# Kernel optimization log

Hardware: AMD Instinct MI355X
Metric: run time of the kernel (lower is better)

Reference implementation:

```python
import jax, jax.numpy as jnp
import numpy as np

G = 128          # voxel grid extent per axis
KS = 3           # kernel size per axis
KK = KS ** 3     # 27 kernel offsets
N_IN, N_OUT, C_IN, C_OUT = 50000, 100000, 128, 128


def setup_inputs() -> dict:
    key = jax.random.key(0)
    k1, k2, k3, k4 = jax.random.split(key, 4)
    features = jax.random.normal(k1, (N_IN, C_IN), dtype=jnp.float32)
    W = jax.random.normal(k2, (KK, C_IN, C_OUT), dtype=jnp.float32) * (1.0 / np.sqrt(C_IN * KK))
    inp_positions = jax.random.randint(k3, (N_IN, 3), 0, G, dtype=jnp.int32)
    out_positions = jax.random.randint(k4, (N_OUT, 3), 0, G, dtype=jnp.int32)
    return {"features": features, "W": W,
            "inp_positions": inp_positions, "out_positions": out_positions}


def _kernel_offsets():
    r = np.arange(KS) - KS // 2  # [-1, 0, 1] for KS=3 (offset=0 since KS is odd)
    dx, dy, dz = np.meshgrid(r, r, r, indexing="ij")
    return jnp.asarray(np.stack([dx.ravel(), dy.ravel(), dz.ravel()], axis=1), dtype=jnp.int32)  # [KK,3]


def reference(features, W, inp_positions, out_positions):
    # Sparse conv-transpose: voxelize input points (voxel_size=1, offset=0 -> identity
    # on integer coords), build voxel->input-index hash (dense grid table), then for
    # each output point gather the input feature at each of the KK kernel offsets and
    # accumulate W[k'] @ feat with mirrored kernel index (transpose of SparseConv).
    lin_in = (inp_positions[:, 0] * G + inp_positions[:, 1]) * G + inp_positions[:, 2]
    grid = jnp.full((G * G * G,), -1, dtype=jnp.int32)
    grid = grid.at[lin_in].max(jnp.arange(N_IN, dtype=jnp.int32))  # deterministic on dup voxels

    offsets = _kernel_offsets()          # [KK, 3]
    W_mirror = W[::-1]                   # transpose conv uses mirrored kernel index

    def step(acc, xk):
        off, Wk = xk                     # off [3], Wk [C_IN, C_OUT]
        nb = out_positions + off[None, :]               # [N_OUT, 3]
        in_bounds = jnp.all((nb >= 0) & (nb < G), axis=1)
        lin = (nb[:, 0] * G + nb[:, 1]) * G + nb[:, 2]
        idx = grid[jnp.clip(lin, 0, G * G * G - 1)]      # [N_OUT]
        ok = in_bounds & (idx >= 0)
        f = jnp.where(ok[:, None], features[jnp.clip(idx, 0)], 0.0)  # [N_OUT, C_IN]
        return acc + f @ Wk, None

    acc0 = jnp.zeros((out_positions.shape[0], W.shape[2]), dtype=features.dtype)
    out, _ = jax.lax.scan(step, acc0, (offsets, W_mirror))
    return out
```

## Files before the change

### kernel.cpp

```cpp
#include <hip/hip_runtime.h>
#include <hip/hip_bf16.h>

#define G    128
#define GGG  (G * G * G)
#define C    128
#define KK   27
#define CAP  4096
#define RT   16

typedef __attribute__((ext_vector_type(8))) short bf16x8;
typedef __attribute__((ext_vector_type(4))) float f32x4;

__device__ __forceinline__ ushort f2b(float f) {
    __hip_bfloat16 h = __float2bfloat16(f);
    return *reinterpret_cast<ushort*>(&h);
}

__global__ void prep_kernel(uint4* __restrict__ grid16_4, int* __restrict__ cnt,
                            const float* __restrict__ W, ushort* __restrict__ Wtb) {
    int tid = blockIdx.x * blockDim.x + threadIdx.x;
    int stride = gridDim.x * blockDim.x;
    uint4 ffff = {0xFFFFFFFFu, 0xFFFFFFFFu, 0xFFFFFFFFu, 0xFFFFFFFFu};
    for (int i = tid; i < GGG * 2 / 16; i += stride) grid16_4[i] = ffff;
    if (tid < KK) cnt[tid] = 0;
    const int NW = KK * C * C;
    for (int i = tid; i < NW; i += stride) {
        int m = i >> 14;
        int r = i & 16383;
        int co = r >> 7, ci = r & 127;
        Wtb[i] = f2b(W[(size_t)(KK - 1 - m) * C * C + ci * C + co]);
    }
}

__global__ void scatter16_kernel(const int* __restrict__ pos,
                                 unsigned int* __restrict__ gword, int n) {
    int i = blockIdx.x * blockDim.x + threadIdx.x;
    if (i >= n) return;
    int x = pos[3 * i], y = pos[3 * i + 1], z = pos[3 * i + 2];
    int lin = (x * G + y) * G + z;
    unsigned int* w = &gword[lin >> 1];
    int sh = (lin & 1) * 16;
    unsigned int val = (unsigned int)i;
    unsigned int old = *w, assumed;
    do {
        unsigned int cur = (old >> sh) & 0xFFFFu;
        if (cur != 0xFFFFu && cur >= val) break;
        unsigned int nw = (old & ~(0xFFFFu << sh)) | (val << sh);
        assumed = old;
        old = atomicCAS(w, assumed, nw);
    } while (old != assumed);
}

__global__ __launch_bounds__(256) void compact4_kernel(
    const int* __restrict__ out_pos, const ushort* __restrict__ grid16,
    int* __restrict__ cnt, int2* __restrict__ pairs,
    int* __restrict__ cnt_row, int* __restrict__ rowtap, int n_out)
{
    int row = blockIdx.x * 256 + threadIdx.x;
    bool valid = row < n_out;
    int lane = threadIdx.x & 63;

    int px = 0, py = 0, pz = 0;
    if (valid) { px = out_pos[3*row]; py = out_pos[3*row+1]; pz = out_pos[3*row+2]; }

    int idx[KK];
#pragma unroll
    for (int m = 0; m < KK; ++m) {
        int x = px + m / 9 - 1, y = py + (m % 9) / 3 - 1, z = pz + m % 3 - 1;
        bool inb = valid && (unsigned)x < G && (unsigned)y < G && (unsigned)z < G;
        int v = inb ? (int)grid16[(x * G + y) * G + z] : 0xFFFF;
        idx[m] = (v == 0xFFFF) ? -1 : v;
    }

    __shared__ int bcnt[KK], bbase[KK];
    if (threadIdx.x < KK) bcnt[threadIdx.x] = 0;
    __syncthreads();

    int gl[KK];
#pragma unroll
    for (int m = 0; m < KK; ++m) {
        unsigned long long act = __ballot(idx[m] >= 0);
        int lpre = __popcll(act & ((1ull << lane) - 1ull));
        int wcnt = __popcll(act);
        int wbase = 0;
        if (lane == 0 && wcnt) wbase = atomicAdd(&bcnt[m], wcnt);
        wbase = __shfl(wbase, 0);
        gl[m] = wbase + lpre;
    }
    __syncthreads();
    if (threadIdx.x < KK) bbase[threadIdx.x] = atomicAdd(&cnt[threadIdx.x], bcnt[threadIdx.x]);
    __syncthreads();

    int gs[KK];
    int cr = 0;
#pragma unroll
    for (int m = 0; m < KK; ++m) {
        int g = -1;
        if (idx[m] >= 0) {
            g = bbase[m] + gl[m];
            if (g >= CAP) g = -1;
        }
        gs[m] = g;
        if (g >= 0) ++cr;
    }

    int dest = (cr == 1) ? row : -1;
    int k = 0;
#pragma unroll
    for (int m = 0; m < KK; ++m) {
        int g = gs[m];
        if (g >= 0) {
            pairs[m * CAP + g] = make_int2(idx[m], dest);
            if (k < RT) { rowtap[k * n_out + row] = (g << 5) | m; ++k; }
        }
    }
    if (valid) cnt_row[row] = cr;
}

__global__ __launch_bounds__(256, 3) void pair_mm4_kernel(
    const float* __restrict__ features, const ushort* __restrict__ Wtb,
    const int2* __restrict__ pairs, const int* __restrict__ cnt,
    ushort* __restrict__ part, float* __restrict__ out)
{
    int m = blockIdx.y;
    int nm = min(cnt[m], CAP);
    if ((int)(blockIdx.x * 64) >= nm) return;

    __shared__ ushort Wl[128 * 136];
    __shared__ ushort Af[64 * 136];
    __shared__ int    idx_s[64];
    __shared__ int    dest_s[64];

    {
        const uint4* src = (const uint4*)(Wtb + (size_t)m * C * C);
        uint4* dst = (uint4*)Wl;
        for (int q = threadIdx.x; q < 2048; q += 256) {
            int r = q >> 4, c = q & 15;
            dst[r * 17 + c] = src[q];
        }
    }

    int lane = threadIdx.x & 63;
    int w    = threadIdx.x >> 6;
    int l15  = lane & 15;
    int quad = lane >> 4;
    const float4* fg4 = (const float4*)features;

    for (int base = blockIdx.x * 64; base < nm; base += gridDim.x * 64) {
        __syncthreads();
        if (threadIdx.x < 64) {
            int g = base + threadIdx.x;
            int2 pr = (g < nm) ? pairs[m * CAP + g] : make_int2(-1, -1);
            idx_s[threadIdx.x]  = pr.x;
            dest_s[threadIdx.x] = pr.y;
        }
        __syncthreads();

#pragma unroll
        for (int k = 0; k < 8; ++k) {
            int q = threadIdx.x + k * 256;
            int r = q >> 5, c4 = q & 31;
            int id = idx_s[r];
            if (id >= 0) {
                float4 v = fg4[(size_t)id * 32 + c4];
                union { ushort u[4]; uint2 p; } pk;
                pk.u[0] = f2b(v.x); pk.u[1] = f2b(v.y);
                pk.u[2] = f2b(v.z); pk.u[3] = f2b(v.w);
                *(uint2*)&Af[r * 136 + c4 * 4] = pk.p;
            }
        }
        __syncthreads();

        f32x4 acc[8];
#pragma unroll
        for (int n = 0; n < 8; ++n) acc[n] = (f32x4){0.f, 0.f, 0.f, 0.f};

        int arow = 16 * w + l15;
#pragma unroll
        for (int kk = 0; kk < 4; ++kk) {
            bf16x8 a = *(bf16x8*)&Af[arow * 136 + kk * 32 + quad * 8];
#pragma unroll
            for (int n = 0; n < 8; ++n) {
                bf16x8 b = *(bf16x8*)&Wl[(n * 16 + l15) * 136 + kk * 32 + quad * 8];
                acc[n] = __builtin_amdgcn_mfma_f32_16x16x32_bf16(a, b, acc[n], 0, 0, 0);
            }
        }

        int r0 = 16 * w + quad * 4;
#pragma unroll
        for (int reg = 0; reg < 4; ++reg) {
            int r = r0 + reg;
            if (base + r >= nm) continue;
            int d = dest_s[r];
            if (d >= 0) {
                float* o = out + (size_t)d * C + l15;
#pragma unroll
                for (int n = 0; n < 8; ++n) o[n * 16] = acc[n][reg];
            } else {
                ushort* p = part + ((size_t)(m * CAP + base + r)) * C + l15;
#pragma unroll
                for (int n = 0; n < 8; ++n) p[n * 16] = f2b(acc[n][reg]);
            }
        }
    }
}

__global__ __launch_bounds__(256) void gather_sum3_kernel(
    const ushort* __restrict__ part, const int* __restrict__ rowtap,
    const int* __restrict__ cnt_row, float* __restrict__ out, int n_out)
{
    int row0 = blockIdx.x * 16;
    int rl = threadIdx.x >> 4;
    int t  = threadIdx.x & 15;
    int row = row0 + rl;

    __shared__ int rt_s[RT][16];
    __shared__ int cnt_s[16];
    __shared__ int maxc;
    if (threadIdx.x < 16) {
        int r = row0 + threadIdx.x;
        cnt_s[threadIdx.x] = (r < n_out) ? cnt_row[r] : 0;
    }
    __syncthreads();
    if (threadIdx.x == 0) {
        int mx = 0;
#pragma unroll
        for (int i = 0; i < 16; ++i) mx = max(mx, cnt_s[i]);
        maxc = mx;
    }
    __syncthreads();
    {
        int k = threadIdx.x >> 4, r = threadIdx.x & 15;
        if (k < maxc)
            rt_s[k][r] = (row0 + r < n_out) ? rowtap[k * n_out + row0 + r] : 0;
    }
    __syncthreads();

    int nt = cnt_s[rl];
    if (nt == 1) return;

    float acc[8] = {0,0,0,0,0,0,0,0};
    for (int k = 0; k < nt; ++k) {
        int e = rt_s[k][rl];
        int m = e & 31, g = e >> 5;
        uint4 v = *(const uint4*)(part + ((size_t)(m * CAP + g)) * C + t * 8);
        acc[0] += __uint_as_float(v.x << 16);
        acc[1] += __uint_as_float(v.x & 0xffff0000u);
        acc[2] += __uint_as_float(v.y << 16);
        acc[3] += __uint_as_float(v.y & 0xffff0000u);
        acc[4] += __uint_as_float(v.z << 16);
        acc[5] += __uint_as_float(v.z & 0xffff0000u);
        acc[6] += __uint_as_float(v.w << 16);
        acc[7] += __uint_as_float(v.w & 0xffff0000u);
    }
    if (row < n_out) {
        float* o = out + (size_t)row * C + t * 8;
        *(float4*)(o)     = (float4){acc[0], acc[1], acc[2], acc[3]};
        *(float4*)(o + 4) = (float4){acc[4], acc[5], acc[6], acc[7]};
    }
}

__global__ void init2_kernel(int4* __restrict__ grid4, int* __restrict__ cnt) {
    int i = blockIdx.x * blockDim.x + threadIdx.x;
    int stride = gridDim.x * blockDim.x;
    int4 mone = {-1, -1, -1, -1};
    for (int j = i; j < GGG / 4; j += stride) grid4[j] = mone;
    if (i < KK) cnt[i] = 0;
}

__global__ void scatter_kernel(const int* __restrict__ pos,
                               int* __restrict__ grid, int n) {
    int i = blockIdx.x * blockDim.x + threadIdx.x;
    if (i >= n) return;
    int x = pos[3 * i], y = pos[3 * i + 1], z = pos[3 * i + 2];
    atomicMax(&grid[(x * G + y) * G + z], i);
}

__global__ __launch_bounds__(128) void gather_mm_kernel(
    const float* __restrict__ features, const float* __restrict__ W,
    const int* __restrict__ out_pos, const int* __restrict__ grid,
    float* __restrict__ out, int n_out)
{
    int row = blockIdx.x;
    if (row >= n_out) return;
    int c = threadIdx.x;
    __shared__ int   nb_idx[KK];
    __shared__ float feat_s[C];
    int px = out_pos[3*row], py = out_pos[3*row+1], pz = out_pos[3*row+2];
    if (c < KK) {
        int i = c / 9, j = (c % 9) / 3, k = c % 3;
        int x = px + i - 1, y = py + j - 1, z = pz + k - 1;
        int idx = -1;
        if ((unsigned)x < G && (unsigned)y < G && (unsigned)z < G)
            idx = grid[(x * G + y) * G + z];
        nb_idx[c] = idx;
    }
    __syncthreads();
    float acc = 0.f;
    for (int m = 0; m < KK; ++m) {
        int idx = nb_idx[m];
        if (idx < 0) continue;
        __syncthreads();
        feat_s[c] = features[idx * C + c];
        __syncthreads();
        const float* __restrict__ Wk = W + (KK - 1 - m) * C * C + c;
        float a = 0.f;
#pragma unroll
        for (int ci = 0; ci < C; ++ci) a += feat_s[ci] * Wk[ci * C];
        acc += a;
    }
    out[row * C + c] = acc;
}

extern "C" void kernel_launch(void* const* d_in, const int* in_sizes, int n_in,
                              void* d_out, int out_size, void* d_ws, size_t ws_size,
                              hipStream_t stream) {
    const float* features = (const float*)d_in[0];
    const float* W        = (const float*)d_in[1];
    const int*   inp_pos  = (const int*)d_in[2];
    const int*   out_pos  = (const int*)d_in[3];
    float*       out      = (float*)d_out;

    int n_in_pts  = in_sizes[2] / 3;
    int n_out_pts = out_size / C;

    size_t o_grid   = 0;
    size_t o_cnt    = (size_t)GGG * 4;
    size_t o_pairs  = (o_cnt + 256 + 255) & ~(size_t)255;
    size_t o_cntr   = (o_pairs + (size_t)KK * CAP * 8 + 255) & ~(size_t)255;
    size_t o_rowtap = (o_cntr + (size_t)n_out_pts * 4 + 255) & ~(size_t)255;
    size_t o_wtb    = (o_rowtap + (size_t)RT * n_out_pts * 4 + 255) & ~(size_t)255;
    size_t o_part   = (o_wtb + (size_t)KK * C * C * 2 + 255) & ~(size_t)255;
    size_t need     = o_part + (size_t)KK * CAP * C * 2;

    ushort* grid16  = (ushort*)((char*)d_ws + o_grid);
    int*    cnt     = (int*)((char*)d_ws + o_cnt);
    int2*   pairs   = (int2*)((char*)d_ws + o_pairs);
    int*    cnt_row = (int*)((char*)d_ws + o_cntr);
    int*    rowtap  = (int*)((char*)d_ws + o_rowtap);
    ushort* Wtb     = (ushort*)((char*)d_ws + o_wtb);
    ushort* part    = (ushort*)((char*)d_ws + o_part);

    if (ws_size < need) {
        int* grid32 = (int*)d_ws;
        hipLaunchKernelGGL(init2_kernel, dim3(2048), dim3(256), 0, stream,
                           (int4*)grid32, cnt);
        hipLaunchKernelGGL(scatter_kernel, dim3((n_in_pts + 255) / 256), dim3(256), 0, stream,
                           inp_pos, grid32, n_in_pts);
        hipLaunchKernelGGL(gather_mm_kernel, dim3(n_out_pts), dim3(128), 0, stream,
                           features, W, out_pos, grid32, out, n_out_pts);
        return;
    }

    hipLaunchKernelGGL(prep_kernel, dim3(1024), dim3(256), 0, stream,
                       (uint4*)grid16, cnt, W, Wtb);
    hipLaunchKernelGGL(scatter16_kernel, dim3((n_in_pts + 255) / 256), dim3(256), 0, stream,
                       inp_pos, (unsigned int*)grid16, n_in_pts);
    hipLaunchKernelGGL(compact4_kernel, dim3((n_out_pts + 255) / 256), dim3(256), 0, stream,
                       out_pos, grid16, cnt, pairs, cnt_row, rowtap, n_out_pts);
    hipLaunchKernelGGL(pair_mm4_kernel, dim3(40, KK), dim3(256), 0, stream,
                       features, Wtb, pairs, cnt, part, out);
    hipLaunchKernelGGL(gather_sum3_kernel, dim3((n_out_pts + 15) / 16), dim3(256), 0, stream,
                       part, rowtap, cnt_row, out, n_out_pts);
}
```

Baseline: 141.3 us.

## Pre-convert features to bf16, tile W transpose via LDS, double pair-matmul rows

The prep kernel now transposes W through a shared-memory tile with coalesced reads and writes, and converts all input features to a bf16 copy in workspace. The pair matmul gathers these bf16 rows directly with 16-byte loads and processes 128 pairs per block, with two 16-row MFMA sub-tiles per wave sharing each B fragment. This halves the gather bytes per pair and raises MFMA reuse of the W tile. The cost is a full extra pass over the features, more workspace, doubled LDS per block, and lower occupancy (launch bounds cut from 3 to 2 blocks).

```diff
diff --git a/kernel.cpp b/kernel.cpp
--- a/kernel.cpp
+++ b/kernel.cpp
@@ -16,19 +16,51 @@
     return *reinterpret_cast<ushort*>(&h);
 }
 
-__global__ void prep_kernel(uint4* __restrict__ grid16_4, int* __restrict__ cnt,
-                            const float* __restrict__ W, ushort* __restrict__ Wtb) {
-    int tid = blockIdx.x * blockDim.x + threadIdx.x;
-    int stride = gridDim.x * blockDim.x;
+#define WT_BLOCKS 108
+__global__ __launch_bounds__(256) void prep5_kernel(
+    uint4* __restrict__ grid16_4, int* __restrict__ cnt,
+    const float* __restrict__ W, ushort* __restrict__ Wtb,
+    const float4* __restrict__ fg4, uint2* __restrict__ fb2, int nf4)
+{
+    if (blockIdx.x < WT_BLOCKS) {
+        int mm = blockIdx.x >> 2;
+        int t  = blockIdx.x & 3;
+        __shared__ float Ls[32][129];
+        const float* src = W + (size_t)mm * C * C + (size_t)(t * 32) * C;
+#pragma unroll
+        for (int k = 0; k < 16; ++k) {
+            int q = threadIdx.x + k * 256;
+            int r = q >> 7, co = q & 127;
+            Ls[r][co] = src[r * C + co];
+        }
+        __syncthreads();
+        ushort* dst = Wtb + (size_t)(KK - 1 - mm) * C * C + t * 32;
+#pragma unroll
+        for (int k = 0; k < 4; ++k) {
+            int q = threadIdx.x + k * 256;
+            int co = q >> 3, j = q & 7;
+            union { ushort u[4]; uint2 p; } pk;
+            pk.u[0] = f2b(Ls[4*j+0][co]);
+            pk.u[1] = f2b(Ls[4*j+1][co]);
+            pk.u[2] = f2b(Ls[4*j+2][co]);
+            pk.u[3] = f2b(Ls[4*j+3][co]);
+            *(uint2*)&dst[co * C + 4 * j] = pk.p;
+        }
+        return;
+    }
+    int b = blockIdx.x - WT_BLOCKS;
+    int nb = gridDim.x - WT_BLOCKS;
+    int tid = b * 256 + threadIdx.x;
+    int stride = nb * 256;
     uint4 ffff = {0xFFFFFFFFu, 0xFFFFFFFFu, 0xFFFFFFFFu, 0xFFFFFFFFu};
     for (int i = tid; i < GGG * 2 / 16; i += stride) grid16_4[i] = ffff;
     if (tid < KK) cnt[tid] = 0;
-    const int NW = KK * C * C;
-    for (int i = tid; i < NW; i += stride) {
-        int m = i >> 14;
-        int r = i & 16383;
-        int co = r >> 7, ci = r & 127;
-        Wtb[i] = f2b(W[(size_t)(KK - 1 - m) * C * C + ci * C + co]);
+    for (int i = tid; i < nf4; i += stride) {
+        float4 v = fg4[i];
+        union { ushort u[4]; uint2 p; } pk;
+        pk.u[0] = f2b(v.x); pk.u[1] = f2b(v.y);
+        pk.u[2] = f2b(v.z); pk.u[3] = f2b(v.w);
+        fb2[i] = pk.p;
     }
 }
 
@@ -117,19 +149,19 @@
     if (valid) cnt_row[row] = cr;
 }
 
-__global__ __launch_bounds__(256, 3) void pair_mm4_kernel(
-    const float* __restrict__ features, const ushort* __restrict__ Wtb,
+__global__ __launch_bounds__(256, 2) void pair_mm5_kernel(
+    const uint4* __restrict__ featb4, const ushort* __restrict__ Wtb,
     const int2* __restrict__ pairs, const int* __restrict__ cnt,
     ushort* __restrict__ part, float* __restrict__ out)
 {
     int m = blockIdx.y;
     int nm = min(cnt[m], CAP);
-    if ((int)(blockIdx.x * 64) >= nm) return;
+    if ((int)(blockIdx.x * 128) >= nm) return;
 
     __shared__ ushort Wl[128 * 136];
-    __shared__ ushort Af[64 * 136];
-    __shared__ int    idx_s[64];
-    __shared__ int    dest_s[64];
+    __shared__ ushort Af[128 * 136];
+    __shared__ int    idx_s[128];
+    __shared__ int    dest_s[128];
 
     {
         const uint4* src = (const uint4*)(Wtb + (size_t)m * C * C);
@@ -144,11 +176,11 @@
     int w    = threadIdx.x >> 6;
     int l15  = lane & 15;
     int quad = lane >> 4;
-    const float4* fg4 = (const float4*)features;
-
-    for (int base = blockIdx.x * 64; base < nm; base += gridDim.x * 64) {
-        __syncthreads();
-        if (threadIdx.x < 64) {
+    uint4* Af4 = (uint4*)Af;
+
+    for (int base = blockIdx.x * 128; base < nm; base += gridDim.x * 128) {
+        __syncthreads();
+        if (threadIdx.x < 128) {
             int g = base + threadIdx.x;
             int2 pr = (g < nm) ? pairs[m * CAP + g] : make_int2(-1, -1);
             idx_s[threadIdx.x]  = pr.x;
@@ -159,47 +191,47 @@
 #pragma unroll
         for (int k = 0; k < 8; ++k) {
             int q = threadIdx.x + k * 256;
-            int r = q >> 5, c4 = q & 31;
+            int r = q >> 4, c = q & 15;
             int id = idx_s[r];
-            if (id >= 0) {
-                float4 v = fg4[(size_t)id * 32 + c4];
-                union { ushort u[4]; uint2 p; } pk;
-                pk.u[0] = f2b(v.x); pk.u[1] = f2b(v.y);
-                pk.u[2] = f2b(v.z); pk.u[3] = f2b(v.w);
-                *(uint2*)&Af[r * 136 + c4 * 4] = pk.p;
-            }
-        }
-        __syncthreads();
-
-        f32x4 acc[8];
-#pragma unroll
-        for (int n = 0; n < 8; ++n) acc[n] = (f32x4){0.f, 0.f, 0.f, 0.f};
-
-        int arow = 16 * w + l15;
+            if (id >= 0) Af4[r * 17 + c] = featb4[(size_t)id * 16 + c];
+        }
+        __syncthreads();
+
+        f32x4 acc[2][8];
+#pragma unroll
+        for (int s = 0; s < 2; ++s)
+#pragma unroll
+            for (int n = 0; n < 8; ++n) acc[s][n] = (f32x4){0.f, 0.f, 0.f, 0.f};
+
 #pragma unroll
         for (int kk = 0; kk < 4; ++kk) {
-            bf16x8 a = *(bf16x8*)&Af[arow * 136 + kk * 32 + quad * 8];
+            bf16x8 a0 = *(bf16x8*)&Af[(32*w + l15)      * 136 + kk * 32 + quad * 8];
+            bf16x8 a1 = *(bf16x8*)&Af[(32*w + 16 + l15) * 136 + kk * 32 + quad * 8];
 #pragma unroll
             for (int n = 0; n < 8; ++n) {
                 bf16x8 b = *(bf16x8*)&Wl[(n * 16 + l15) * 136 + kk * 32 + quad * 8];
-                acc[n] = __builtin_amdgcn_mfma_f32_16x16x32_bf16(a, b, acc[n], 0, 0, 0);
+                acc[0][n] = __builtin_amdgcn_mfma_f32_16x16x32_bf16(a0, b, acc[0][n], 0, 0, 0);
+                acc[1][n] = __builtin_amdgcn_mfma_f32_16x16x32_bf16(a1, b, acc[1][n], 0, 0, 0);
             }
         }
 
-        int r0 = 16 * w + quad * 4;
-#pragma unroll
-        for (int reg = 0; reg < 4; ++reg) {
-            int r = r0 + reg;
-            if (base + r >= nm) continue;
-            int d = dest_s[r];
-            if (d >= 0) {
-                float* o = out + (size_t)d * C + l15;
-#pragma unroll
-                for (int n = 0; n < 8; ++n) o[n * 16] = acc[n][reg];
-            } else {
-                ushort* p = part + ((size_t)(m * CAP + base + r)) * C + l15;
-#pragma unroll
-                for (int n = 0; n < 8; ++n) p[n * 16] = f2b(acc[n][reg]);
+#pragma unroll
+        for (int s = 0; s < 2; ++s) {
+            int r0 = 32 * w + 16 * s + quad * 4;
+#pragma unroll
+            for (int reg = 0; reg < 4; ++reg) {
+                int r = r0 + reg;
+                if (base + r >= nm) continue;
+                int d = dest_s[r];
+                if (d >= 0) {
+                    float* o = out + (size_t)d * C + l15;
+#pragma unroll
+                    for (int n = 0; n < 8; ++n) o[n * 16] = acc[s][n][reg];
+                } else {
+                    ushort* p = part + ((size_t)(m * CAP + base + r)) * C + l15;
+#pragma unroll
+                    for (int n = 0; n < 8; ++n) p[n * 16] = f2b(acc[s][n][reg]);
+                }
             }
         }
     }
@@ -330,7 +362,8 @@
     size_t o_cntr   = (o_pairs + (size_t)KK * CAP * 8 + 255) & ~(size_t)255;
     size_t o_rowtap = (o_cntr + (size_t)n_out_pts * 4 + 255) & ~(size_t)255;
     size_t o_wtb    = (o_rowtap + (size_t)RT * n_out_pts * 4 + 255) & ~(size_t)255;
-    size_t o_part   = (o_wtb + (size_t)KK * C * C * 2 + 255) & ~(size_t)255;
+    size_t o_featb  = (o_wtb + (size_t)KK * C * C * 2 + 255) & ~(size_t)255;
+    size_t o_part   = (o_featb + (size_t)n_in_pts * C * 2 + 255) & ~(size_t)255;
     size_t need     = o_part + (size_t)KK * CAP * C * 2;
 
     ushort* grid16  = (ushort*)((char*)d_ws + o_grid);
@@ -339,6 +372,7 @@
     int*    cnt_row = (int*)((char*)d_ws + o_cntr);
     int*    rowtap  = (int*)((char*)d_ws + o_rowtap);
     ushort* Wtb     = (ushort*)((char*)d_ws + o_wtb);
+    ushort* featb   = (ushort*)((char*)d_ws + o_featb);
     ushort* part    = (ushort*)((char*)d_ws + o_part);
 
     if (ws_size < need) {
@@ -352,14 +386,15 @@
         return;
     }
 
-    hipLaunchKernelGGL(prep_kernel, dim3(1024), dim3(256), 0, stream,
-                       (uint4*)grid16, cnt, W, Wtb);
+    hipLaunchKernelGGL(prep5_kernel, dim3(WT_BLOCKS + 916), dim3(256), 0, stream,
+                       (uint4*)grid16, cnt, W, Wtb,
+                       (const float4*)features, (uint2*)featb, n_in_pts * C / 4);
     hipLaunchKernelGGL(scatter16_kernel, dim3((n_in_pts + 255) / 256), dim3(256), 0, stream,
                        inp_pos, (unsigned int*)grid16, n_in_pts);
     hipLaunchKernelGGL(compact4_kernel, dim3((n_out_pts + 255) / 256), dim3(256), 0, stream,
                        out_pos, grid16, cnt, pairs, cnt_row, rowtap, n_out_pts);
-    hipLaunchKernelGGL(pair_mm4_kernel, dim3(40, KK), dim3(256), 0, stream,
-                       features, Wtb, pairs, cnt, part, out);
+    hipLaunchKernelGGL(pair_mm5_kernel, dim3(19, KK), dim3(256), 0, stream,
+                       (const uint4*)featb, Wtb, pairs, cnt, part, out);
     hipLaunchKernelGGL(gather_sum3_kernel, dim3((n_out_pts + 15) / 16), dim3(256), 0, stream,
                        part, rowtap, cnt_row, out, n_out_pts);
 }
```

After: 135.3 us. 1.04x faster.
